# Performance work log

Measured on AMD Instinct MI355X. Metric: run time of the kernel, lower is better.

The kernel has to match this reference:

```python
import jax, jax.numpy as jnp
import numpy as np
import math

D, H, F = 1024, 16, 4096
DH = D // H
EPS_LN = 1e-5


def _layernorm(x, scale, bias):
    mu = jnp.mean(x, axis=-1, keepdims=True)
    var = jnp.mean(jnp.square(x - mu), axis=-1, keepdims=True)
    return (x - mu) * jax.lax.rsqrt(var + EPS_LN) * scale + bias


def setup_inputs() -> dict:
    key = jax.random.key(0)
    ks = jax.random.split(key, 16)
    B, T = 2, 2048
    src = jax.random.normal(ks[0], (B, T, D), dtype=jnp.float32)
    attn_mask = jax.random.randint(ks[1], (T, T), 0, 2) == 1  # bool [T,S], True = masked
    xavier = lambda k, shp: jax.random.uniform(k, shp, jnp.float32, -1.0, 1.0) * math.sqrt(6.0 / (shp[0] + shp[1]))
    return {
        "src": src, "attn_mask": attn_mask,
        "q_w": xavier(ks[2], (D, D)), "q_b": jnp.zeros((D,), jnp.float32),
        "k_w": xavier(ks[3], (D, D)), "k_b": jnp.zeros((D,), jnp.float32),
        "v_w": xavier(ks[4], (D, D)), "v_b": jnp.zeros((D,), jnp.float32),
        "o_w": xavier(ks[5], (D, D)), "o_b": jnp.zeros((D,), jnp.float32),
        "l1_w": xavier(ks[6], (F, D)), "l1_b": jnp.zeros((F,), jnp.float32),
        "l2_w": xavier(ks[7], (D, F)), "l2_b": jnp.zeros((D,), jnp.float32),
        "n1_s": jnp.ones((D,), jnp.float32), "n1_b": jnp.zeros((D,), jnp.float32),
        "n2_s": jnp.ones((D,), jnp.float32), "n2_b": jnp.zeros((D,), jnp.float32),
        "alpha_attn": jax.random.normal(ks[8], (), jnp.float32) * 0.1,
        "alpha_ff": jax.random.normal(ks[9], (), jnp.float32) * 0.1,
    }


def reference(src, attn_mask, q_w, q_b, k_w, k_b, v_w, v_b, o_w, o_b,
              l1_w, l1_b, l2_w, l2_b, n1_s, n1_b, n2_s, n2_b,
              alpha_attn, alpha_ff):
    B, T, _ = src.shape
    # --- self-attention block (post-norm layer, dropout=0 => identity) ---
    q = (src @ q_w.T + q_b).reshape(B, T, H, DH).transpose(0, 2, 1, 3)  # [B,H,T,DH]
    k = (src @ k_w.T + k_b).reshape(B, T, H, DH).transpose(0, 2, 1, 3)
    v = (src @ v_w.T + v_b).reshape(B, T, H, DH).transpose(0, 2, 1, 3)
    scores = jnp.einsum('bhtd,bhsd->bhts', q, k) / math.sqrt(DH)  # [B,H,T,S]
    scores = jnp.where(attn_mask[None, None, :, :], -jnp.inf, scores)
    probs = jax.nn.softmax(scores + 1e-9, axis=-1)
    probs = jnp.where(jnp.isinf(scores), 0.0, probs)  # zero where masked (custom semantics)
    attn = jnp.einsum('bhts,bhsd->bhtd', probs, v).transpose(0, 2, 1, 3).reshape(B, T, D)
    attn = attn @ o_w.T + o_b
    x = _layernorm(src + alpha_attn * attn, n1_s, n1_b)
    # --- FFN block ---
    ff = jax.nn.relu(x @ l1_w.T + l1_b) @ l2_w.T + l2_b
    x = _layernorm(x + alpha_ff * ff, n2_s, n2_b)
    return x
```

## Files before the change

### kernel.cpp

```cpp
#include <hip/hip_runtime.h>
#include <math.h>

#define Dm 1024
#define Hh 16
#define DHd 64
#define Ff 4096
#define Tt 2048
#define Bb 2

#define ATT_C2 0.18033688011112042f

typedef __bf16 bf16_8 __attribute__((ext_vector_type(8)));
typedef __bf16 bf16x2 __attribute__((ext_vector_type(2)));
typedef __bf16 bf16x4 __attribute__((ext_vector_type(4)));
typedef float  f32x4  __attribute__((ext_vector_type(4)));
typedef float  f32x16 __attribute__((ext_vector_type(16)));
typedef unsigned int u32x4 __attribute__((ext_vector_type(4)));
typedef unsigned int u32x8s __attribute__((ext_vector_type(8)));

__device__ __forceinline__ unsigned short f2bf(float f) {
    unsigned int u = __float_as_uint(f);
    unsigned int r = (u + 0x7fffu + ((u >> 16) & 1u)) >> 16;
    return (unsigned short)r;
}

__device__ __forceinline__ bf16x2 pkbf(float a, float b) {
#if __has_builtin(__builtin_amdgcn_cvt_pk_bf16_f32)
    return __builtin_amdgcn_cvt_pk_bf16_f32(a, b);
#else
    bf16x2 r; r[0] = (__bf16)a; r[1] = (__bf16)b; return r;
#endif
}
__device__ __forceinline__ bf16x4 pkbf4(float a, float b, float c, float d) {
    bf16x2 lo = pkbf(a, b), hi = pkbf(c, d);
    return __builtin_shufflevector(lo, hi, 0, 1, 2, 3);
}

__device__ __forceinline__ void plswap32(unsigned &a, unsigned &b) {
#if __has_builtin(__builtin_amdgcn_permlane32_swap)
    auto r = __builtin_amdgcn_permlane32_swap((int)a, (int)b, false, false);
    a = (unsigned)r[0]; b = (unsigned)r[1];
#else
    asm volatile("v_permlane32_swap_b32 %0, %1" : "+v"(a), "+v"(b));
#endif
}

__device__ __forceinline__ void gld_lds16(const void* g, void* l) {
    __builtin_amdgcn_global_load_lds(
        (const __attribute__((address_space(1))) void*)g,
        (__attribute__((address_space(3))) void*)l,
        16, 0, 0);
}

__device__ __forceinline__ void sload32(const unsigned* p,
        u32x8s &a, u32x8s &b, u32x8s &c, u32x8s &d) {
    asm volatile(
        "s_load_dwordx8 %0, %4, 0x0\n\t"
        "s_load_dwordx8 %1, %4, 0x20\n\t"
        "s_load_dwordx8 %2, %4, 0x40\n\t"
        "s_load_dwordx8 %3, %4, 0x60\n\t"
        "s_waitcnt lgkmcnt(0)"
        : "=&s"(a), "=&s"(b), "=&s"(c), "=&s"(d)
        : "s"(p));
}

__device__ __forceinline__ float selkeep(float e, unsigned long long keep) {
    float r;
    asm("v_cndmask_b32 %0, 0, %1, %2" : "=v"(r) : "v"(e), "s"(keep));
    return r;
}

__global__ __launch_bounds__(256) void preprocess_kernel(
    const float* __restrict__ q_w, const float* __restrict__ k_w,
    const float* __restrict__ v_w, const float* __restrict__ o_w,
    const float* __restrict__ l1_w, const float* __restrict__ l2_w,
    const float* __restrict__ src, const int* __restrict__ mask,
    const float* __restrict__ q_b, const float* __restrict__ k_b,
    unsigned short* __restrict__ qkw, unsigned short* __restrict__ vw16,
    unsigned short* __restrict__ ow,  unsigned short* __restrict__ l1w,
    unsigned short* __restrict__ l2w, unsigned short* __restrict__ srcb,
    unsigned* __restrict__ mbT, float* __restrict__ qkb)
{
    const int bid = blockIdx.x;
    const int tid = threadIdx.x;
    if (bid < 16384) {
        int i = bid * 256 + tid;
        const float* sp; unsigned short* dp; int off;
        if (i < 1048576) {
            if (i < 262144)      { sp = q_w; dp = qkw;           off = i; }
            else if (i < 524288) { sp = k_w; dp = qkw + 1048576; off = i - 262144; }
            else if (i < 786432) { sp = v_w; dp = vw16;          off = i - 524288; }
            else                 { sp = o_w; dp = ow;            off = i - 786432; }
        } else if (i < 2097152)  { sp = l1_w; dp = l1w;          off = i - 1048576; }
        else if (i < 3145728)    { sp = l2_w; dp = l2w;          off = i - 2097152; }
        else                     { sp = src;  dp = srcb;         off = i - 3145728; }
        float4 v = ((const float4*)sp)[off];
        ((bf16x4*)dp)[off] = pkbf4(v.x, v.y, v.z, v.w);
    } else if (bid < 16896) {
        int w = (bid - 16384) * 256 + tid;
        int tw32 = w >> 11, s = w & 2047;
        const int* p = mask + (size_t)(tw32 * 32) * 2048 + s;
        unsigned bits = 0;
        #pragma unroll
        for (int j = 0; j < 32; ++j)
            bits |= (p[(size_t)j * 2048] == 0 ? 1u : 0u) << j;
        mbT[w] = bits;
    } else {
        int i = (bid - 16896) * 256 + tid;
        qkb[i] = (i < 1024) ? q_b[i] : k_b[i - 1024];
    }
}

__global__ __launch_bounds__(512, 4) void gemm_splitk8_kernel(
    const unsigned short* __restrict__ A, const unsigned short* __restrict__ W,
    const float* __restrict__ bias, float* __restrict__ C, float* __restrict__ C2,
    int K, int ldc, int ksub)
{
    __shared__ __align__(16) char smem[65536];
    __bf16* As = (__bf16*)smem;
    __bf16* Bs = (__bf16*)(smem + 32768);

    const int tid  = threadIdx.x;
    const int lane = tid & 63;
    const int wave = tid >> 6;
    const int wvu  = __builtin_amdgcn_readfirstlane(wave);
    const int wq   = wvu & 3;
    const int kh   = wvu >> 2;
    const int m0 = blockIdx.y * 128;
    const int n0 = blockIdx.x * 128;
    const int wm = (wq & 1) * 64;
    const int wn = (wq >> 1) * 64;
    const int quad = lane >> 4;
    const int lm = lane & 15;
    const int z  = blockIdx.z;
    const int kstart = z * ksub;
    float* Cz = (z == 0) ? C : C2;

    const int lr4 = lane >> 4;
    const int lc  = lane & 15;

    f32x4 acc[4][4];
    #pragma unroll
    for (int i = 0; i < 4; i++)
        #pragma unroll
        for (int j = 0; j < 4; j++) {
            acc[i][j][0] = 0.f; acc[i][j][1] = 0.f;
            acc[i][j][2] = 0.f; acc[i][j][3] = 0.f;
        }

    for (int k0 = kstart; k0 < kstart + ksub; k0 += 128) {
        __syncthreads();
        #pragma unroll
        for (int i = 0; i < 4; ++i) {
            int seg = wave * 4 + i;
            int r = seg * 4 + lr4;
            int ch = lc ^ (r & 7);
            gld_lds16(A + (size_t)(m0 + r) * K + k0 + ch * 8, &As[seg * 512]);
            gld_lds16(W + (size_t)(n0 + r) * K + k0 + ch * 8, &Bs[seg * 512]);
        }
        __syncthreads();
        #pragma unroll
        for (int kk = 0; kk < 2; ++kk) {
            bf16_8 af[4], bfr[4];
            #pragma unroll
            for (int t = 0; t < 4; ++t) {
                int ra = wm + t * 16 + lm;
                int ca = (kh * 8 + kk * 4 + quad) ^ (ra & 7);
                af[t]  = *(const bf16_8*)&As[ra * 128 + ca * 8];
                int rb = wn + t * 16 + lm;
                int cb = (kh * 8 + kk * 4 + quad) ^ (rb & 7);
                bfr[t] = *(const bf16_8*)&Bs[rb * 128 + cb * 8];
            }
            #pragma unroll
            for (int i = 0; i < 4; i++)
                #pragma unroll
                for (int j = 0; j < 4; j++)
                    acc[i][j] = __builtin_amdgcn_mfma_f32_16x16x32_bf16(
                        af[i], bfr[j], acc[i][j], 0, 0, 0);
        }
    }

    __syncthreads();
    float* comb = (float*)smem;
    if (kh == 1) {
        #pragma unroll
        for (int i = 0; i < 4; i++)
            #pragma unroll
            for (int j = 0; j < 4; j++)
                *(f32x4*)&comb[wq * 4096 + (i * 4 + j) * 256 + lane * 4] =
                    acc[i][j];
    }
    __syncthreads();
    if (kh == 0) {
        float bvc[4];
        #pragma unroll
        for (int j = 0; j < 4; j++)
            bvc[j] = (z == 0) ? bias[n0 + wn + j * 16 + lm] : 0.f;
        #pragma unroll
        for (int i = 0; i < 4; i++)
            #pragma unroll
            for (int j = 0; j < 4; j++) {
                f32x4 v4 = *(const f32x4*)&comb[
                    wq * 4096 + (i * 4 + j) * 256 + lane * 4];
                int col = n0 + wn + j * 16 + lm;
                #pragma unroll
                for (int r = 0; r < 4; r++) {
                    int row = m0 + wm + i * 16 + quad * 4 + r;
                    Cz[(size_t)row * ldc + col] = acc[i][j][r] + v4[r] + bvc[j];
                }
            }
    }
}

__global__ __launch_bounds__(256, 2) void gemm_ffn1_kernel(
    const unsigned short* __restrict__ A, const unsigned short* __restrict__ W,
    const float* __restrict__ bias, unsigned short* __restrict__ C)
{
    __shared__ __bf16 As[256][64];
    __shared__ __bf16 Bs[128][64];
    const int tid  = threadIdx.x;
    const int lane = tid & 63;
    const int wave = tid >> 6;
    const int m0 = blockIdx.y * 256;
    const int n0 = blockIdx.x * 128;
    const int lr8 = lane >> 3;
    const int gch = (lane & 7) ^ lr8;
    const int quad = lane >> 4;
    const int lm = lane & 15;

    f32x4 acc[4][8];
    #pragma unroll
    for (int i = 0; i < 4; i++)
        #pragma unroll
        for (int j = 0; j < 8; j++) {
            acc[i][j][0] = 0.f; acc[i][j][1] = 0.f;
            acc[i][j][2] = 0.f; acc[i][j][3] = 0.f;
        }

    for (int k0 = 0; k0 < 1024; k0 += 64) {
        __syncthreads();
        #pragma unroll
        for (int i = 0; i < 8; i++) {
            int seg = wave * 8 + i;
            int r = seg * 8 + lr8;
            gld_lds16(A + (size_t)(m0 + r) * 1024 + k0 + gch * 8, &As[seg * 8][0]);
        }
        #pragma unroll
        for (int i = 0; i < 4; i++) {
            int seg = wave * 4 + i;
            int r = seg * 8 + lr8;
            gld_lds16(W + (size_t)(n0 + r) * 1024 + k0 + gch * 8, &Bs[seg * 8][0]);
        }
        __syncthreads();
        #pragma unroll
        for (int kh = 0; kh < 2; kh++) {
            const int ch = (kh * 4 + quad) ^ (lm & 7);
            bf16_8 af[4], bfr[8];
            #pragma unroll
            for (int t = 0; t < 4; t++)
                af[t] = *(const bf16_8*)&As[wave * 64 + t * 16 + lm][ch * 8];
            #pragma unroll
            for (int j = 0; j < 8; j++)
                bfr[j] = *(const bf16_8*)&Bs[j * 16 + lm][ch * 8];
            #pragma unroll
            for (int i = 0; i < 4; i++)
                #pragma unroll
                for (int j = 0; j < 8; j++)
                    acc[i][j] = __builtin_amdgcn_mfma_f32_16x16x32_bf16(
                        af[i], bfr[j], acc[i][j], 0, 0, 0);
        }
    }

    float bv[8];
    #pragma unroll
    for (int j = 0; j < 8; j++) bv[j] = bias[n0 + j * 16 + lm];

    #pragma unroll
    for (int i = 0; i < 4; i++)
        #pragma unroll
        for (int j = 0; j < 8; j++) {
            int col = n0 + j * 16 + lm;
            #pragma unroll
            for (int r = 0; r < 4; r++) {
                int row = m0 + wave * 64 + i * 16 + quad * 4 + r;
                float v = fmaxf(acc[i][j][r] + bv[j], 0.f);
                C[(size_t)row * Ff + col] = f2bf(v);
            }
        }
}

__global__ __launch_bounds__(256) void gemm_qkvt_kernel(
    const unsigned short* __restrict__ srcb, const unsigned short* __restrict__ qkw,
    const unsigned short* __restrict__ vw16, const float* __restrict__ qkb,
    const float* __restrict__ v_b,
    unsigned short* __restrict__ qk16, unsigned short* __restrict__ vtf)
{
    const int bid = blockIdx.x;
    const unsigned short *A, *W;
    const float* bias;
    unsigned short* C;
    int m0, n0, ldc;
    bool qscale, rowbias;
    if (bid < 512) {
        A = srcb; W = qkw; bias = qkb; C = qk16;
        n0 = (bid & 15) * 128; m0 = (bid >> 4) * 128;
        ldc = 2048; qscale = true; rowbias = false;
    } else {
        int b2 = bid - 512;
        A = vw16; W = srcb; bias = v_b; C = vtf;
        n0 = (b2 & 31) * 128; m0 = (b2 >> 5) * 128;
        ldc = 4096; qscale = false; rowbias = true;
    }
    const int K = 1024;

    __shared__ __bf16 As[128][64];
    __shared__ __bf16 Bs[128][64];
    const int tid  = threadIdx.x;
    const int lane = tid & 63;
    const int wave = tid >> 6;
    const int lr8 = lane >> 3;
    const int gch = (lane & 7) ^ lr8;
    const int wm = (wave & 1) * 64;
    const int wn = (wave >> 1) * 64;
    const int quad = lane >> 4;
    const int lm = lane & 15;

    f32x4 acc[4][4];
    #pragma unroll
    for (int i = 0; i < 4; i++)
        #pragma unroll
        for (int j = 0; j < 4; j++) {
            acc[i][j][0] = 0.f; acc[i][j][1] = 0.f;
            acc[i][j][2] = 0.f; acc[i][j][3] = 0.f;
        }

    for (int k0 = 0; k0 < K; k0 += 64) {
        __syncthreads();
        #pragma unroll
        for (int i = 0; i < 4; i++) {
            int seg = wave * 4 + i;
            int r = seg * 8 + lr8;
            gld_lds16(A + (size_t)(m0 + r) * K + k0 + gch * 8, &As[seg * 8][0]);
            gld_lds16(W + (size_t)(n0 + r) * K + k0 + gch * 8, &Bs[seg * 8][0]);
        }
        __syncthreads();
        #pragma unroll
        for (int kh = 0; kh < 2; kh++) {
            bf16_8 af[4], bfr[4];
            #pragma unroll
            for (int t = 0; t < 4; t++) {
                int ch = (kh * 4 + quad) ^ (lm & 7);
                af[t]  = *(const bf16_8*)&As[wm + t * 16 + lm][ch * 8];
                bfr[t] = *(const bf16_8*)&Bs[wn + t * 16 + lm][ch * 8];
            }
            #pragma unroll
            for (int i = 0; i < 4; i++)
                #pragma unroll
                for (int j = 0; j < 4; j++)
                    acc[i][j] = __builtin_amdgcn_mfma_f32_16x16x32_bf16(
                        af[i], bfr[j], acc[i][j], 0, 0, 0);
        }
    }

    float bvc[4];
    float brr[4][4];
    if (!rowbias) {
        #pragma unroll
        for (int j = 0; j < 4; j++) bvc[j] = bias[n0 + wn + j * 16 + lm];
    } else {
        #pragma unroll
        for (int i = 0; i < 4; i++) {
            float4 t4 = *(const float4*)&bias[m0 + wm + i * 16 + quad * 4];
            brr[i][0] = t4.x; brr[i][1] = t4.y; brr[i][2] = t4.z; brr[i][3] = t4.w;
        }
    }

    #pragma unroll
    for (int i = 0; i < 4; i++)
        #pragma unroll
        for (int j = 0; j < 4; j++) {
            int col = n0 + wn + j * 16 + lm;
            #pragma unroll
            for (int r = 0; r < 4; r++) {
                int row = m0 + wm + i * 16 + quad * 4 + r;
                float v = acc[i][j][r] + (rowbias ? brr[i][r] : bvc[j]);
                if (qscale && col < 1024) v *= ATT_C2;
                C[(size_t)row * ldc + col] = f2bf(v);
            }
        }
}

__global__ __launch_bounds__(512, 4) void attn_mfma_kernel(
    const unsigned short* __restrict__ qk,
    const unsigned short* __restrict__ vt,
    const unsigned* __restrict__ mbT,
    unsigned short* __restrict__ out)
{
    __shared__ __align__(16) char smem[65536];
    __bf16* KsP = (__bf16*)smem;
    __bf16* VtP = (__bf16*)(smem + 32768);

    const int tid  = threadIdx.x;
    const int lane = tid & 63;
    const int wave = tid >> 6;
    const int l31  = lane & 31;
    const int hi   = lane >> 5;
    const int x7   = l31 & 7;
    const int bh = blockIdx.y;
    const int b = bh >> 4, h = bh & 15;
    const int wvu = __builtin_amdgcn_readfirstlane(wave);
    const int wq  = wvu & 3;
    const int sh  = wvu >> 2;
    const int tw = blockIdx.x * 128 + wq * 32;
    const unsigned* mrow = mbT + (size_t)(blockIdx.x * 4 + wq) * 2048;

    bf16_8 qf[4];
    #pragma unroll
    for (int ds4 = 0; ds4 < 4; ++ds4)
        qf[ds4] = *(const bf16_8*)(qk +
            (size_t)(b * Tt + tw + l31) * 2048 + h * DHd + ds4 * 16 + hi * 8);

    f32x16 oacc[2];
    f32x16 ol;
    f32x16 z16;
    #pragma unroll
    for (int r = 0; r < 16; ++r) {
        oacc[0][r] = 0.f; oacc[1][r] = 0.f; ol[r] = 0.f; z16[r] = 0.f;
    }
    bf16_8 vone;
    {
        __bf16 one = (__bf16)1.0f;
        #pragma unroll
        for (int j = 0; j < 8; ++j) vone[j] = one;
    }

    const int krow8 = lane >> 3;
    const int kj    = (lane & 7) ^ krow8;
    const int vr4   = lane >> 4;

    auto STAGE = [&](int nb, int s0) {
        #pragma unroll
        for (int i = 0; i < 2; ++i) {
            int ci = wave * 2 + i;
            {
                int r = 8 * ci + krow8;
                const unsigned short* g = qk +
                    (size_t)(b * Tt + s0 + r) * 2048 + 1024 + h * DHd + kj * 8;
                gld_lds16(g, &KsP[nb * 8192 + ci * 512]);
            }
            {
                int d = 4 * ci + vr4;
                int jj = (lane & 15) ^ (d & 7);
                const unsigned short* g = vt +
                    (size_t)(h * DHd + d) * 4096 + b * Tt + s0 + jj * 8;
                gld_lds16(g, &VtP[nb * 8192 + ci * 512]);
            }
        }
    };

    STAGE(0, 0);

    for (int st = 0; st < 16; ++st) {
        const int cb = st & 1;
        const int s0 = st * 128;
        __syncthreads();

        if (st < 15) STAGE(cb ^ 1, s0 + 128);

        #pragma unroll
        for (int sbl = 0; sbl < 2; ++sbl) {
            const int sb = sh * 2 + sbl;
            u32x8s ma, mbw, mc, md;
            sload32(mrow + s0 + sb * 32, ma, mbw, mc, md);

            f32x16 sacc = z16;
            #pragma unroll
            for (int ds4 = 0; ds4 < 4; ++ds4) {
                bf16_8 kf = *(const bf16_8*)&KsP[cb * 8192 +
                    (sb * 32 + l31) * 64 + (((ds4 * 2 + hi) ^ x7) * 8)];
                sacc = __builtin_amdgcn_mfma_f32_32x32x16_bf16(
                    kf, qf[ds4], sacc, 0, 0, 0);
            }
            float p[16];
            #pragma unroll
            for (int g = 0; g < 4; ++g) {
                u32x8s vv = (g == 0) ? ma : (g == 1) ? mbw : (g == 2) ? mc : md;
                #pragma unroll
                for (int m = 0; m < 4; ++m) {
                    const int reg = g * 4 + m;
                    unsigned long long keep =
                        ((unsigned long long)vv[m + 4] << 32) |
                        (unsigned long long)vv[m];
                    float e = __builtin_amdgcn_exp2f(sacc[reg]);
                    p[reg] = selkeep(e, keep);
                }
            }
            unsigned u[4], v[4];
            #pragma unroll
            for (int g = 0; g < 4; ++g) {
                u[g] = __builtin_bit_cast(unsigned, pkbf(p[g * 4 + 0], p[g * 4 + 1]));
                v[g] = __builtin_bit_cast(unsigned, pkbf(p[g * 4 + 2], p[g * 4 + 3]));
            }
            plswap32(u[0], u[1]); plswap32(v[0], v[1]);
            plswap32(u[2], u[3]); plswap32(v[2], v[3]);
            u32x4 w0; w0[0] = u[0]; w0[1] = v[0]; w0[2] = u[1]; w0[3] = v[1];
            u32x4 w1; w1[0] = u[2]; w1[1] = v[2]; w1[2] = u[3]; w1[3] = v[3];
            bf16_8 pa0 = __builtin_bit_cast(bf16_8, w0);
            bf16_8 pa1 = __builtin_bit_cast(bf16_8, w1);
            #pragma unroll
            for (int kst = 0; kst < 2; ++kst) {
                bf16_8 pa = kst ? pa1 : pa0;
                #pragma unroll
                for (int dblk = 0; dblk < 2; ++dblk) {
                    int cpos = (sb * 4 + kst * 2 + hi) ^ x7;
                    bf16_8 vf = *(const bf16_8*)&VtP[cb * 8192 +
                        ((dblk * 32 + l31) * 16 + cpos) * 8];
                    oacc[dblk] = __builtin_amdgcn_mfma_f32_32x32x16_bf16(
                        pa, vf, oacc[dblk], 0, 0, 0);
                }
                ol = __builtin_amdgcn_mfma_f32_32x32x16_bf16(
                    pa, vone, ol, 0, 0, 0);
            }
        }
    }

    __syncthreads();
    float* comb = (float*)smem;
    if (sh == 1) {
        #pragma unroll
        for (int dblk = 0; dblk < 2; ++dblk)
            #pragma unroll
            for (int q = 0; q < 4; ++q) {
                float4 v4 = { oacc[dblk][q * 4 + 0], oacc[dblk][q * 4 + 1],
                              oacc[dblk][q * 4 + 2], oacc[dblk][q * 4 + 3] };
                *(float4*)&comb[wq * 3072 + (dblk * 4 + q) * 256 + lane * 4] = v4;
            }
        #pragma unroll
        for (int q = 0; q < 4; ++q) {
            float4 v4 = { ol[q * 4 + 0], ol[q * 4 + 1],
                          ol[q * 4 + 2], ol[q * 4 + 3] };
            *(float4*)&comb[wq * 3072 + (8 + q) * 256 + lane * 4] = v4;
        }
    }
    __syncthreads();
    if (sh == 0) {
        #pragma unroll
        for (int dblk = 0; dblk < 2; ++dblk)
            #pragma unroll
            for (int q = 0; q < 4; ++q) {
                float4 v4 = *(const float4*)&comb[
                    wq * 3072 + (dblk * 4 + q) * 256 + lane * 4];
                oacc[dblk][q * 4 + 0] += v4.x; oacc[dblk][q * 4 + 1] += v4.y;
                oacc[dblk][q * 4 + 2] += v4.z; oacc[dblk][q * 4 + 3] += v4.w;
            }
        #pragma unroll
        for (int q = 0; q < 4; ++q) {
            float4 v4 = *(const float4*)&comb[
                wq * 3072 + (8 + q) * 256 + lane * 4];
            ol[q * 4 + 0] += v4.x; ol[q * 4 + 1] += v4.y;
            ol[q * 4 + 2] += v4.z; ol[q * 4 + 3] += v4.w;
        }
        #pragma unroll
        for (int g = 0; g < 4; ++g)
            #pragma unroll
            for (int m = 0; m < 4; ++m) {
                const int reg = g * 4 + m;
                const int tr = m + 8 * g + 4 * hi;
                float l = ol[reg];
                float inv = (l > 0.f) ? 1.f / l : 0.f;
                int row = b * Tt + tw + tr;
                #pragma unroll
                for (int dblk = 0; dblk < 2; ++dblk)
                    out[(size_t)row * Dm + h * DHd + dblk * 32 + l31] =
                        f2bf(oacc[dblk][reg] * inv);
            }
    }
}

template<int NPARTS, int BASEBF, int OUTF32, int OUTBF>
__global__ __launch_bounds__(256) void residual_ln_kernel(
    const void* __restrict__ base, const float* __restrict__ d0,
    const float* __restrict__ d1,
    const float* __restrict__ alpha_p, const float* __restrict__ scale,
    const float* __restrict__ bias, float* __restrict__ out,
    unsigned short* __restrict__ out_bf)
{
    const int row = blockIdx.x;
    const int tid = threadIdx.x;
    const float alpha = alpha_p[0];
    float4 xb;
    if (BASEBF) {
        bf16x4 bb = ((const bf16x4*)((const unsigned short*)base + (size_t)row * Dm))[tid];
        xb.x = (float)bb[0]; xb.y = (float)bb[1]; xb.z = (float)bb[2]; xb.w = (float)bb[3];
    } else {
        xb = ((const float4*)((const float*)base + (size_t)row * Dm))[tid];
    }
    float4 xd = ((const float4*)(d0 + (size_t)row * Dm))[tid];
    if (NPARTS == 2) {
        float4 x2 = ((const float4*)(d1 + (size_t)row * Dm))[tid];
        xd.x += x2.x; xd.y += x2.y; xd.z += x2.z; xd.w += x2.w;
    }
    float4 x;
    x.x = xb.x + alpha * xd.x;
    x.y = xb.y + alpha * xd.y;
    x.z = xb.z + alpha * xd.z;
    x.w = xb.w + alpha * xd.w;
    float s  = x.x + x.y + x.z + x.w;
    float sq = x.x*x.x + x.y*x.y + x.z*x.z + x.w*x.w;
    #pragma unroll
    for (int off = 32; off > 0; off >>= 1) {
        s  += __shfl_down(s, off, 64);
        sq += __shfl_down(sq, off, 64);
    }
    __shared__ float red[8];
    const int w = tid >> 6;
    if ((tid & 63) == 0) { red[w] = s; red[4 + w] = sq; }
    __syncthreads();
    s  = red[0] + red[1] + red[2] + red[3];
    sq = red[4] + red[5] + red[6] + red[7];
    const float mu  = s * (1.f / Dm);
    const float var = sq * (1.f / Dm) - mu * mu;
    const float r   = rsqrtf(var + 1e-5f);
    float4 sc = ((const float4*)scale)[tid];
    float4 bi = ((const float4*)bias)[tid];
    float4 o;
    o.x = (x.x - mu) * r * sc.x + bi.x;
    o.y = (x.y - mu) * r * sc.y + bi.y;
    o.z = (x.z - mu) * r * sc.z + bi.z;
    o.w = (x.w - mu) * r * sc.w + bi.w;
    if (OUTF32)
        ((float4*)(out + (size_t)row * Dm))[tid] = o;
    if (OUTBF)
        ((bf16x4*)(out_bf + (size_t)row * Dm))[tid] = pkbf4(o.x, o.y, o.z, o.w);
}

extern "C" void kernel_launch(void* const* d_in, const int* in_sizes, int n_in,
                              void* d_out, int out_size, void* d_ws, size_t ws_size,
                              hipStream_t stream)
{
    (void)in_sizes; (void)n_in; (void)out_size; (void)ws_size;
    const float* src  = (const float*)d_in[0];
    const int*   mask = (const int*)  d_in[1];
    const float* q_w  = (const float*)d_in[2];
    const float* q_b  = (const float*)d_in[3];
    const float* k_w  = (const float*)d_in[4];
    const float* k_b  = (const float*)d_in[5];
    const float* v_w  = (const float*)d_in[6];
    const float* v_b  = (const float*)d_in[7];
    const float* o_w  = (const float*)d_in[8];
    const float* o_b  = (const float*)d_in[9];
    const float* l1_w = (const float*)d_in[10];
    const float* l1_b = (const float*)d_in[11];
    const float* l2_w = (const float*)d_in[12];
    const float* l2_b = (const float*)d_in[13];
    const float* n1_s = (const float*)d_in[14];
    const float* n1_b = (const float*)d_in[15];
    const float* n2_s = (const float*)d_in[16];
    const float* n2_b = (const float*)d_in[17];
    const float* a_attn = (const float*)d_in[18];
    const float* a_ff   = (const float*)d_in[19];

    const size_t MB = 1024 * 1024;
    char* w = (char*)d_ws;
    unsigned short* qkw  = (unsigned short*)(w + 0);
    unsigned short* vw16 = (unsigned short*)(w + 4  * MB);
    unsigned short* ow   = (unsigned short*)(w + 6  * MB);
    unsigned short* l1w  = (unsigned short*)(w + 8  * MB);
    unsigned short* l2w  = (unsigned short*)(w + 16 * MB);
    unsigned short* srcb = (unsigned short*)(w + 24 * MB);
    unsigned short* qk16 = (unsigned short*)(w + 32 * MB);
    unsigned short* vtf  = (unsigned short*)(w + 48 * MB);
    unsigned*       mbT  = (unsigned*)      (w + 56 * MB);
    float*          qkb  = (float*)         (w + 56 * MB + 524288);
    unsigned short* atb  = (unsigned short*)(w + 24 * MB);
    float*          o0   = (float*)         (w + 58 * MB);
    float*          o1   = (float*)         (w + 74 * MB);
    unsigned short* x1b  = (unsigned short*)(w + 48 * MB);
    unsigned short* hb   = (unsigned short*)(w + 58 * MB);
    float*          fp0  = (float*)         (w + 0);
    float*          fp1  = (float*)         (w + 32 * MB);

    const int MR = Bb * Tt;
    dim3 blk(256);

    preprocess_kernel<<<dim3(16904), blk, 0, stream>>>(
        q_w, k_w, v_w, o_w, l1_w, l2_w, src, mask, q_b, k_b,
        qkw, vw16, ow, l1w, l2w, srcb, mbT, qkb);
    gemm_qkvt_kernel<<<dim3(768), blk, 0, stream>>>(
        srcb, qkw, vw16, qkb, v_b, qk16, vtf);
    attn_mfma_kernel<<<dim3(16, 32), dim3(512), 0, stream>>>(qk16, vtf, mbT, atb);
    gemm_splitk8_kernel<<<dim3(8, 32, 2), dim3(512), 0, stream>>>(
        atb, ow, o_b, o0, o1, Dm, Dm, 512);
    residual_ln_kernel<2, 0, 0, 1><<<dim3(MR), blk, 0, stream>>>(
        src, o0, o1, a_attn, n1_s, n1_b, nullptr, x1b);
    gemm_ffn1_kernel<<<dim3(32, 16), blk, 0, stream>>>(x1b, l1w, l1_b, hb);
    gemm_splitk8_kernel<<<dim3(8, 32, 2), dim3(512), 0, stream>>>(
        hb, l2w, l2_b, fp0, fp1, Ff, Dm, 2048);
    residual_ln_kernel<2, 1, 1, 0><<<dim3(MR), blk, 0, stream>>>(
        x1b, fp0, fp1, a_ff, n2_s, n2_b, (float*)d_out, nullptr);
}
```

Before: 356.2 us.

## Split attention KV tile four ways per block and drop LDS double buffering

Each attention block now handles 64 query rows instead of 128. Its 8 waves are split as 2 query groups by 4 key sub-blocks, so every wave processes one 32-key sub-block per 128-key stage. LDS is halved by removing the double-buffered K/V staging, which lets more blocks be resident, and the launch-bounds hint goes from 4 to 8. The grid doubles and the partial sums are combined through a multi-round LDS reduction. In exchange, the kernel gains an extra barrier per stage, loses load/compute overlap, and reloads each K/V tile twice as often.

```diff
diff --git a/kernel.cpp b/kernel.cpp
--- a/kernel.cpp
+++ b/kernel.cpp
@@ -390,15 +390,15 @@
         }
 }
 
-__global__ __launch_bounds__(512, 4) void attn_mfma_kernel(
+__global__ __launch_bounds__(512, 8) void attn_mfma_kernel(
     const unsigned short* __restrict__ qk,
     const unsigned short* __restrict__ vt,
     const unsigned* __restrict__ mbT,
     unsigned short* __restrict__ out)
 {
-    __shared__ __align__(16) char smem[65536];
+    __shared__ __align__(16) char smem[32768];
     __bf16* KsP = (__bf16*)smem;
-    __bf16* VtP = (__bf16*)(smem + 32768);
+    __bf16* VtP = (__bf16*)(smem + 16384);
 
     const int tid  = threadIdx.x;
     const int lane = tid & 63;
@@ -409,10 +409,10 @@
     const int bh = blockIdx.y;
     const int b = bh >> 4, h = bh & 15;
     const int wvu = __builtin_amdgcn_readfirstlane(wave);
-    const int wq  = wvu & 3;
-    const int sh  = wvu >> 2;
-    const int tw = blockIdx.x * 128 + wq * 32;
-    const unsigned* mrow = mbT + (size_t)(blockIdx.x * 4 + wq) * 2048;
+    const int wq  = wvu & 1;
+    const int sh  = wvu >> 1;
+    const int tw = blockIdx.x * 64 + wq * 32;
+    const unsigned* mrow = mbT + (size_t)(blockIdx.x * 2 + wq) * 2048;
 
     bf16_8 qf[4];
     #pragma unroll
@@ -438,7 +438,10 @@
     const int kj    = (lane & 7) ^ krow8;
     const int vr4   = lane >> 4;
 
-    auto STAGE = [&](int nb, int s0) {
+    for (int st = 0; st < 16; ++st) {
+        const int s0 = st * 128;
+        __syncthreads();
+
         #pragma unroll
         for (int i = 0; i < 2; ++i) {
             int ci = wave * 2 + i;
@@ -446,120 +449,120 @@
                 int r = 8 * ci + krow8;
                 const unsigned short* g = qk +
                     (size_t)(b * Tt + s0 + r) * 2048 + 1024 + h * DHd + kj * 8;
-                gld_lds16(g, &KsP[nb * 8192 + ci * 512]);
+                gld_lds16(g, &KsP[ci * 512]);
             }
             {
                 int d = 4 * ci + vr4;
                 int jj = (lane & 15) ^ (d & 7);
                 const unsigned short* g = vt +
                     (size_t)(h * DHd + d) * 4096 + b * Tt + s0 + jj * 8;
-                gld_lds16(g, &VtP[nb * 8192 + ci * 512]);
-            }
-        }
+                gld_lds16(g, &VtP[ci * 512]);
+            }
+        }
+        __syncthreads();
+
+        const int sb = sh;
+        u32x8s ma, mbw, mc, md;
+        sload32(mrow + s0 + sb * 32, ma, mbw, mc, md);
+
+        f32x16 sacc = z16;
+        #pragma unroll
+        for (int ds4 = 0; ds4 < 4; ++ds4) {
+            bf16_8 kf = *(const bf16_8*)&KsP[
+                (sb * 32 + l31) * 64 + (((ds4 * 2 + hi) ^ x7) * 8)];
+            sacc = __builtin_amdgcn_mfma_f32_32x32x16_bf16(
+                kf, qf[ds4], sacc, 0, 0, 0);
+        }
+        float p[16];
+        #pragma unroll
+        for (int g = 0; g < 4; ++g) {
+            u32x8s vv = (g == 0) ? ma : (g == 1) ? mbw : (g == 2) ? mc : md;
+            #pragma unroll
+            for (int m = 0; m < 4; ++m) {
+                const int reg = g * 4 + m;
+                unsigned long long keep =
+                    ((unsigned long long)vv[m + 4] << 32) |
+                    (unsigned long long)vv[m];
+                float e = __builtin_amdgcn_exp2f(sacc[reg]);
+                p[reg] = selkeep(e, keep);
+            }
+        }
+        unsigned u[4], v[4];
+        #pragma unroll
+        for (int g = 0; g < 4; ++g) {
+            u[g] = __builtin_bit_cast(unsigned, pkbf(p[g * 4 + 0], p[g * 4 + 1]));
+            v[g] = __builtin_bit_cast(unsigned, pkbf(p[g * 4 + 2], p[g * 4 + 3]));
+        }
+        plswap32(u[0], u[1]); plswap32(v[0], v[1]);
+        plswap32(u[2], u[3]); plswap32(v[2], v[3]);
+        u32x4 w0; w0[0] = u[0]; w0[1] = v[0]; w0[2] = u[1]; w0[3] = v[1];
+        u32x4 w1; w1[0] = u[2]; w1[1] = v[2]; w1[2] = u[3]; w1[3] = v[3];
+        bf16_8 pa0 = __builtin_bit_cast(bf16_8, w0);
+        bf16_8 pa1 = __builtin_bit_cast(bf16_8, w1);
+        #pragma unroll
+        for (int kst = 0; kst < 2; ++kst) {
+            bf16_8 pa = kst ? pa1 : pa0;
+            #pragma unroll
+            for (int dblk = 0; dblk < 2; ++dblk) {
+                int cpos = (sb * 4 + kst * 2 + hi) ^ x7;
+                bf16_8 vf = *(const bf16_8*)&VtP[
+                    ((dblk * 32 + l31) * 16 + cpos) * 8];
+                oacc[dblk] = __builtin_amdgcn_mfma_f32_32x32x16_bf16(
+                    pa, vf, oacc[dblk], 0, 0, 0);
+            }
+            ol = __builtin_amdgcn_mfma_f32_32x32x16_bf16(
+                pa, vone, ol, 0, 0, 0);
+        }
+    }
+
+    auto getp = [&](int pi) {
+        f32x4 v4;
+        #pragma unroll
+        for (int r = 0; r < 4; ++r)
+            v4[r] = (pi < 4) ? oacc[0][pi * 4 + r]
+                  : (pi < 8) ? oacc[1][(pi - 4) * 4 + r]
+                             : ol[(pi - 8) * 4 + r];
+        return v4;
     };
-
-    STAGE(0, 0);
-
-    for (int st = 0; st < 16; ++st) {
-        const int cb = st & 1;
-        const int s0 = st * 128;
-        __syncthreads();
-
-        if (st < 15) STAGE(cb ^ 1, s0 + 128);
-
-        #pragma unroll
-        for (int sbl = 0; sbl < 2; ++sbl) {
-            const int sb = sh * 2 + sbl;
-            u32x8s ma, mbw, mc, md;
-            sload32(mrow + s0 + sb * 32, ma, mbw, mc, md);
-
-            f32x16 sacc = z16;
-            #pragma unroll
-            for (int ds4 = 0; ds4 < 4; ++ds4) {
-                bf16_8 kf = *(const bf16_8*)&KsP[cb * 8192 +
-                    (sb * 32 + l31) * 64 + (((ds4 * 2 + hi) ^ x7) * 8)];
-                sacc = __builtin_amdgcn_mfma_f32_32x32x16_bf16(
-                    kf, qf[ds4], sacc, 0, 0, 0);
-            }
-            float p[16];
-            #pragma unroll
-            for (int g = 0; g < 4; ++g) {
-                u32x8s vv = (g == 0) ? ma : (g == 1) ? mbw : (g == 2) ? mc : md;
-                #pragma unroll
-                for (int m = 0; m < 4; ++m) {
-                    const int reg = g * 4 + m;
-                    unsigned long long keep =
-                        ((unsigned long long)vv[m + 4] << 32) |
-                        (unsigned long long)vv[m];
-                    float e = __builtin_amdgcn_exp2f(sacc[reg]);
-                    p[reg] = selkeep(e, keep);
-                }
-            }
-            unsigned u[4], v[4];
-            #pragma unroll
-            for (int g = 0; g < 4; ++g) {
-                u[g] = __builtin_bit_cast(unsigned, pkbf(p[g * 4 + 0], p[g * 4 + 1]));
-                v[g] = __builtin_bit_cast(unsigned, pkbf(p[g * 4 + 2], p[g * 4 + 3]));
-            }
-            plswap32(u[0], u[1]); plswap32(v[0], v[1]);
-            plswap32(u[2], u[3]); plswap32(v[2], v[3]);
-            u32x4 w0; w0[0] = u[0]; w0[1] = v[0]; w0[2] = u[1]; w0[3] = v[1];
-            u32x4 w1; w1[0] = u[2]; w1[1] = v[2]; w1[2] = u[3]; w1[3] = v[3];
-            bf16_8 pa0 = __builtin_bit_cast(bf16_8, w0);
-            bf16_8 pa1 = __builtin_bit_cast(bf16_8, w1);
-            #pragma unroll
-            for (int kst = 0; kst < 2; ++kst) {
-                bf16_8 pa = kst ? pa1 : pa0;
-                #pragma unroll
-                for (int dblk = 0; dblk < 2; ++dblk) {
-                    int cpos = (sb * 4 + kst * 2 + hi) ^ x7;
-                    bf16_8 vf = *(const bf16_8*)&VtP[cb * 8192 +
-                        ((dblk * 32 + l31) * 16 + cpos) * 8];
-                    oacc[dblk] = __builtin_amdgcn_mfma_f32_32x32x16_bf16(
-                        pa, vf, oacc[dblk], 0, 0, 0);
-                }
-                ol = __builtin_amdgcn_mfma_f32_32x32x16_bf16(
-                    pa, vone, ol, 0, 0, 0);
-            }
-        }
-    }
-
+    auto addp = [&](int pi, f32x4 v4) {
+        #pragma unroll
+        for (int r = 0; r < 4; ++r) {
+            if (pi < 4)      oacc[0][pi * 4 + r] += v4[r];
+            else if (pi < 8) oacc[1][(pi - 4) * 4 + r] += v4[r];
+            else             ol[(pi - 8) * 4 + r] += v4[r];
+        }
+    };
     __syncthreads();
     float* comb = (float*)smem;
-    if (sh == 1) {
-        #pragma unroll
-        for (int dblk = 0; dblk < 2; ++dblk)
-            #pragma unroll
-            for (int q = 0; q < 4; ++q) {
-                float4 v4 = { oacc[dblk][q * 4 + 0], oacc[dblk][q * 4 + 1],
-                              oacc[dblk][q * 4 + 2], oacc[dblk][q * 4 + 3] };
-                *(float4*)&comb[wq * 3072 + (dblk * 4 + q) * 256 + lane * 4] = v4;
-            }
-        #pragma unroll
-        for (int q = 0; q < 4; ++q) {
-            float4 v4 = { ol[q * 4 + 0], ol[q * 4 + 1],
-                          ol[q * 4 + 2], ol[q * 4 + 3] };
-            *(float4*)&comb[wq * 3072 + (8 + q) * 256 + lane * 4] = v4;
-        }
+    #pragma unroll
+    for (int hf = 0; hf < 2; ++hf) {
+        if (sh & 1) {
+            int slot = wq * 2 + (sh >> 1);
+            #pragma unroll
+            for (int pi = 0; pi < 6; ++pi)
+                *(f32x4*)&comb[slot * 1536 + pi * 256 + lane * 4] =
+                    getp(hf * 6 + pi);
+        }
+        __syncthreads();
+        if (!(sh & 1)) {
+            int slot = wq * 2 + (sh >> 1);
+            #pragma unroll
+            for (int pi = 0; pi < 6; ++pi)
+                addp(hf * 6 + pi,
+                     *(const f32x4*)&comb[slot * 1536 + pi * 256 + lane * 4]);
+        }
+        __syncthreads();
+    }
+    if (sh == 2) {
+        #pragma unroll
+        for (int pi = 0; pi < 12; ++pi)
+            *(f32x4*)&comb[wq * 3072 + pi * 256 + lane * 4] = getp(pi);
     }
     __syncthreads();
     if (sh == 0) {
         #pragma unroll
-        for (int dblk = 0; dblk < 2; ++dblk)
-            #pragma unroll
-            for (int q = 0; q < 4; ++q) {
-                float4 v4 = *(const float4*)&comb[
-                    wq * 3072 + (dblk * 4 + q) * 256 + lane * 4];
-                oacc[dblk][q * 4 + 0] += v4.x; oacc[dblk][q * 4 + 1] += v4.y;
-                oacc[dblk][q * 4 + 2] += v4.z; oacc[dblk][q * 4 + 3] += v4.w;
-            }
-        #pragma unroll
-        for (int q = 0; q < 4; ++q) {
-            float4 v4 = *(const float4*)&comb[
-                wq * 3072 + (8 + q) * 256 + lane * 4];
-            ol[q * 4 + 0] += v4.x; ol[q * 4 + 1] += v4.y;
-            ol[q * 4 + 2] += v4.z; ol[q * 4 + 3] += v4.w;
-        }
+        for (int pi = 0; pi < 12; ++pi)
+            addp(pi, *(const f32x4*)&comb[wq * 3072 + pi * 256 + lane * 4]);
         #pragma unroll
         for (int g = 0; g < 4; ++g)
             #pragma unroll
@@ -688,7 +691,7 @@
         qkw, vw16, ow, l1w, l2w, srcb, mbT, qkb);
     gemm_qkvt_kernel<<<dim3(768), blk, 0, stream>>>(
         srcb, qkw, vw16, qkb, v_b, qk16, vtf);
-    attn_mfma_kernel<<<dim3(16, 32), dim3(512), 0, stream>>>(qk16, vtf, mbT, atb);
+    attn_mfma_kernel<<<dim3(32, 32), dim3(512), 0, stream>>>(qk16, vtf, mbT, atb);
     gemm_splitk8_kernel<<<dim3(8, 32, 2), dim3(512), 0, stream>>>(
         atb, ow, o_b, o0, o1, Dm, Dm, 512);
     residual_ln_kernel<2, 0, 0, 1><<<dim3(MR), blk, 0, stream>>>(
```

New measurement: 1.211 ms. 3.4x slower.
